# Kernel tuning notes

Hardware: AMD Instinct MI355X
Metric: run time of the kernel (lower is better)

Reference implementation:

```python
import jax, jax.numpy as jnp
import numpy as np

B, T, SLATE, D = 256, 16, 20, 256
N_ITEMS, N_USERS = 100000, 10000


def setup_inputs() -> dict:
    key = jax.random.key(0)
    ks = jax.random.split(key, 8)
    s = 1.0 / np.sqrt(D)  # PyTorch GRU/Linear init scale ~ U(-1/sqrt(H), 1/sqrt(H))
    return {
        "item_idxs": jax.random.randint(ks[0], (B, T, SLATE), 0, N_ITEMS),
        "user_idxs": jax.random.randint(ks[1], (B, T), 0, N_USERS),
        "responses": jnp.zeros((B, T, SLATE), jnp.float32),
        "item_table": jax.random.normal(ks[2], (N_ITEMS, D), jnp.float32) * 0.02,
        "user_table": jax.random.normal(ks[3], (N_USERS, D), jnp.float32) * 0.02,
        "W_ih": jax.random.uniform(ks[4], (3 * D, 2 * D), jnp.float32, -s, s),
        "W_hh": jax.random.uniform(ks[5], (3 * D, D), jnp.float32, -s, s),
        "b_ih": jnp.zeros((3 * D,), jnp.float32),
        "b_hh": jnp.zeros((3 * D,), jnp.float32),
        "W_out": jax.random.uniform(ks[6], (1, D), jnp.float32, -s, s),
        "b_out": jnp.zeros((1,), jnp.float32),
    }


def _gru_cell(x, h, W_ih, W_hh, b_ih, b_hh):
    # PyTorch GRUCell math. x: [N, 2D], h: [N, D]
    gi = x @ W_ih.T + b_ih  # [N, 3D]
    gh = h @ W_hh.T + b_hh  # [N, 3D]
    i_r, i_z, i_n = jnp.split(gi, 3, axis=-1)
    h_r, h_z, h_n = jnp.split(gh, 3, axis=-1)
    r = jax.nn.sigmoid(i_r + h_r)
    z = jax.nn.sigmoid(i_z + h_z)
    n = jnp.tanh(i_n + r * h_n)
    return (1.0 - z) * n + z * h


def reference(item_idxs, user_idxs, responses, item_table, user_table,
              W_ih, W_hh, b_ih, b_hh, W_out, b_out):
    # embedding lookup: item_embs [B,T,S,D], user_embs [B,T,D]
    item_embs = item_table[item_idxs]
    user_embs = user_table[user_idxs]
    N = B * T
    e = item_embs.reshape(N, SLATE, D).transpose(1, 0, 2)  # [S, N, D]
    h0 = user_embs.reshape(N, D)
    m0 = jnp.ones((N, 1), item_embs.dtype)  # 'soft' readout multiplier, 1 at step 0

    def step(carry, e_i):
        h, m = carry
        x = jnp.concatenate([e_i, e_i * m], axis=-1)  # [N, 2D]
        h = _gru_cell(x, h, W_ih, W_hh, b_ih, b_hh)
        y = h @ W_out.T + b_out  # [N, 1]
        return (h, jax.nn.sigmoid(y)), y[:, 0]

    _, ys = jax.lax.scan(step, (h0, m0), e)  # ys: [S, N]
    return ys.transpose(1, 0).reshape(B, T, SLATE)
```

## Files before the change

### kernel.cpp

```cpp
#include <hip/hip_runtime.h>
#include <math.h>

#define SLATE 20
#define DD 256
#define NSEQ 4096

typedef __attribute__((ext_vector_type(8))) short bf16x8;
typedef __attribute__((ext_vector_type(4))) float f32x4;
typedef unsigned short u16;
typedef unsigned int u32;

__device__ __forceinline__ u16 f2bf(float f) {
    unsigned u = __float_as_uint(f);
    u += 0x7fff + ((u >> 16) & 1);
    return (u16)(u >> 16);
}
__device__ __forceinline__ float blo(u32 u) { return __uint_as_float(u << 16); }
__device__ __forceinline__ float bhi(u32 u) { return __uint_as_float(u & 0xffff0000u); }
__device__ __forceinline__ float sigm_(float x) {
    return __builtin_amdgcn_rcpf(1.f + __builtin_amdgcn_exp2f(-1.44269504f * x));
}
__device__ __forceinline__ float tanh_(float x) {
    return 1.f - 2.f * __builtin_amdgcn_rcpf(1.f + __builtin_amdgcn_exp2f(2.88539008f * x));
}

__device__ __forceinline__ void gl_lds16(const void* g, void* l) {
    __builtin_amdgcn_global_load_lds(
        (const __attribute__((address_space(1))) unsigned int*)g,
        (__attribute__((address_space(3))) unsigned int*)l, 16, 0, 0);
}

__global__ void prep_w(const float* __restrict__ W_ih, const float* __restrict__ W_hh,
                       u16* __restrict__ W12, u16* __restrict__ Whh) {
    int i = blockIdx.x * 256 + threadIdx.x;
    if (i < 1536 * 256) {
        int j = i >> 8, k = i & 255;
        float v = (j < 768) ? W_ih[(size_t)j * 512 + k]
                            : W_ih[(size_t)(j - 768) * 512 + 256 + k];
        W12[i] = f2bf(v);
    } else {
        int i2 = i - 1536 * 256;
        Whh[i2] = f2bf(W_hh[i2]);
    }
}

__global__ void gather_e(int s0, const int* __restrict__ idxs, const float* __restrict__ itab,
                         u16* __restrict__ e_bf) {
    int g = blockIdx.x * 256 + threadIdx.x;
    int row = g >> 6, c = g & 63;
    int n = row & (NSEQ - 1), s = s0 + (row >> 12);
    int idx = idxs[n * SLATE + s];
    float4 v = *(const float4*)&itab[(size_t)idx * DD + c * 4];
    ushort4 o;
    o.x = f2bf(v.x); o.y = f2bf(v.y); o.z = f2bf(v.z); o.w = f2bf(v.w);
    *(ushort4*)&e_bf[(size_t)row * DD + c * 4] = o;
}

__global__ __launch_bounds__(256) void gemm_e(
        const u16* __restrict__ e_bf, const u16* __restrict__ W12,
        const float* __restrict__ b_ih, u16* __restrict__ Ge) {
    __shared__ u16 A_s[128][32];
    __shared__ u16 B_s[128][32];

    const int tid = threadIdx.x;
    const int w = tid >> 6, l = tid & 63, lm = l & 15, lq = l >> 4;
    const int wm = w & 1, wn = w >> 1;
    const size_t m0 = (size_t)blockIdx.y * 128;
    const size_t n0 = (size_t)blockIdx.x * 128;

    f32x4 acc[4][4];
    f32x4 zero4 = {0.f, 0.f, 0.f, 0.f};
#pragma unroll
    for (int mi = 0; mi < 4; ++mi)
#pragma unroll
        for (int nj = 0; nj < 4; ++nj) acc[mi][nj] = zero4;

    const int srow = w * 16 + (l >> 2);
    const int skc = (l & 3) * 8;
    const u16* gA = e_bf + (m0 + srow) * DD + skc;
    const u16* gB = W12 + (n0 + srow) * DD + skc;
    u16* lA = &A_s[0][0] + w * 512 + l * 8;
    u16* lB = &B_s[0][0] + w * 512 + l * 8;

    for (int kt = 0; kt < 8; ++kt) {
        const int ko = kt * 32;
        gl_lds16(gA + ko, lA);
        gl_lds16(gA + 64 * DD + ko, lA + 2048);
        gl_lds16(gB + ko, lB);
        gl_lds16(gB + 64 * DD + ko, lB + 2048);
        __syncthreads();
        bf16x8 af[4], bfr[4];
#pragma unroll
        for (int mi = 0; mi < 4; ++mi)
            af[mi] = *(const bf16x8*)&A_s[wm * 64 + mi * 16 + lm][lq * 8];
#pragma unroll
        for (int nj = 0; nj < 4; ++nj)
            bfr[nj] = *(const bf16x8*)&B_s[wn * 64 + nj * 16 + lm][lq * 8];
#pragma unroll
        for (int nj = 0; nj < 4; ++nj)
#pragma unroll
            for (int mi = 0; mi < 4; ++mi)
                acc[mi][nj] = __builtin_amdgcn_mfma_f32_16x16x32_bf16(af[mi], bfr[nj], acc[mi][nj], 0, 0, 0);
        __syncthreads();
    }
    float bb[4];
#pragma unroll
    for (int nj = 0; nj < 4; ++nj) {
        int col = (int)n0 + wn * 64 + nj * 16 + lm;
        bb[nj] = (col < 768) ? b_ih[col] : 0.f;
    }
#pragma unroll
    for (int mi = 0; mi < 4; ++mi)
#pragma unroll
        for (int rr = 0; rr < 4; ++rr) {
            u16* gp = Ge + (m0 + wm * 64 + mi * 16 + lq * 4 + rr) * 1536 + n0 + wn * 64 + lm;
#pragma unroll
            for (int nj = 0; nj < 4; ++nj) gp[nj * 16] = f2bf(acc[mi][nj][rr] + bb[nj]);
        }
}

__device__ __forceinline__ int hA_off(int seq, int kt, int lq2) {
    int v = ((kt & 3) << 2) | lq2;
    return kt * 512 + lq2 * 128 + ((seq ^ v) << 3);
}

__global__ __launch_bounds__(1024, 4) void seq_kernel(
        int s0, int C,
        const u16* __restrict__ Ge,
        const u16* __restrict__ Whh,
        const int* __restrict__ user_idxs, const float* __restrict__ user_table,
        const float* __restrict__ b_hh,
        const float* __restrict__ W_out, const float* __restrict__ b_out,
        float* __restrict__ h_g, float* __restrict__ m_g, float* __restrict__ out)
{
    __shared__ u16   hA[4096];
    __shared__ float gh_s[16][770];

    const int tid = threadIdx.x;
    const int w = tid >> 6, l = tid & 63, lm = l & 15, lq = l >> 4;
    const int n0 = blockIdx.x * 16;
    const int nw = n0 + w;
    const int jw = w * 48;

    const u16* wbase = Whh + (size_t)(jw + lm) * DD + lq * 8;
    bf16x8 warr0[8], warr1[8];
#pragma unroll
    for (int kt = 0; kt < 8; ++kt) {
        warr0[kt] = *(const bf16x8*)(wbase + kt * 32);
        warr1[kt] = *(const bf16x8*)(wbase + 16 * DD + kt * 32);
    }
    const u16* wb2 = wbase + 32 * DD;

    float bhh0 = b_hh[jw + lm], bhh1 = b_hh[jw + 16 + lm], bhh2 = b_hh[jw + 32 + lm];
    float2 woA = *(const float2*)&W_out[2 * l];
    float2 woB = *(const float2*)&W_out[2 * l + 128];
    const float bo = b_out[0];

    float h_reg[4]; float m_w;
    if (s0 == 0) {
        const float* hu = user_table + (size_t)user_idxs[nw] * DD;
        float2 a = *(const float2*)&hu[2 * l];
        float2 b = *(const float2*)&hu[2 * l + 128];
        h_reg[0] = a.x; h_reg[1] = a.y; h_reg[2] = b.x; h_reg[3] = b.y; m_w = 1.f;
    } else {
        float2 a = *(const float2*)&h_g[(size_t)nw * DD + 2 * l];
        float2 b = *(const float2*)&h_g[(size_t)nw * DD + 2 * l + 128];
        h_reg[0] = a.x; h_reg[1] = a.y; h_reg[2] = b.x; h_reg[3] = b.y; m_w = m_g[nw];
    }
#pragma unroll
    for (int c = 0; c < 2; ++c) {
        int kt = (l >> 4) + 4 * c, lq2 = (l >> 2) & 3;
        u32 pk = (u32)f2bf(h_reg[2 * c]) | ((u32)f2bf(h_reg[2 * c + 1]) << 16);
        *(u32*)&hA[hA_off(w, kt, lq2) + 2 * (l & 3)] = pk;
    }
    __syncthreads();

    for (int sc = 0; sc < C; ++sc) {
        u32 ge2[2][6];
        const u32* geb = (const u32*)(Ge + ((size_t)sc * NSEQ + nw) * 1536);
#pragma unroll
        for (int c = 0; c < 2; ++c)
#pragma unroll
            for (int g = 0; g < 6; ++g)
                ge2[c][g] = geb[g * 128 + l + 64 * c];

        f32x4 zero4 = {0.f, 0.f, 0.f, 0.f};
        f32x4 acc0 = zero4, acc1 = zero4, acc2 = zero4;
#pragma unroll
        for (int kt = 0; kt < 8; ++kt) {
            bf16x8 af = *(const bf16x8*)&hA[hA_off(lm, kt, lq)];
            acc0 = __builtin_amdgcn_mfma_f32_16x16x32_bf16(af, warr0[kt], acc0, 0, 0, 0);
            acc1 = __builtin_amdgcn_mfma_f32_16x16x32_bf16(af, warr1[kt], acc1, 0, 0, 0);
            bf16x8 b2 = *(const bf16x8*)(wb2 + kt * 32);
            acc2 = __builtin_amdgcn_mfma_f32_16x16x32_bf16(af, b2, acc2, 0, 0, 0);
        }
#pragma unroll
        for (int rr = 0; rr < 4; ++rr) {
            gh_s[lq * 4 + rr][jw + lm]      = acc0[rr] + bhh0;
            gh_s[lq * 4 + rr][jw + 16 + lm] = acc1[rr] + bhh1;
            gh_s[lq * 4 + rr][jw + 32 + lm] = acc2[rr] + bhh2;
        }
        __syncthreads();

        float yv = 0.f;
#pragma unroll
        for (int c = 0; c < 2; ++c) {
            const int d0 = 2 * l + 128 * c;
            float2 ghr = *(const float2*)&gh_s[w][d0];
            float2 ghz = *(const float2*)&gh_s[w][256 + d0];
            float2 ghn = *(const float2*)&gh_s[w][512 + d0];
            float ir_lo = fmaf(m_w, blo(ge2[c][3]), blo(ge2[c][0]));
            float ir_hi = fmaf(m_w, bhi(ge2[c][3]), bhi(ge2[c][0]));
            float iz_lo = fmaf(m_w, blo(ge2[c][4]), blo(ge2[c][1]));
            float iz_hi = fmaf(m_w, bhi(ge2[c][4]), bhi(ge2[c][1]));
            float in_lo = fmaf(m_w, blo(ge2[c][5]), blo(ge2[c][2]));
            float in_hi = fmaf(m_w, bhi(ge2[c][5]), bhi(ge2[c][2]));
            float r_lo = sigm_(ir_lo + ghr.x);
            float r_hi = sigm_(ir_hi + ghr.y);
            float z_lo = sigm_(iz_lo + ghz.x);
            float z_hi = sigm_(iz_hi + ghz.y);
            float n_lo = tanh_(fmaf(r_lo, ghn.x, in_lo));
            float n_hi = tanh_(fmaf(r_hi, ghn.y, in_hi));
            float hn_lo = fmaf(z_lo, h_reg[2 * c] - n_lo, n_lo);
            float hn_hi = fmaf(z_hi, h_reg[2 * c + 1] - n_hi, n_hi);
            h_reg[2 * c] = hn_lo; h_reg[2 * c + 1] = hn_hi;
            int kt = (l >> 4) + 4 * c, lq2 = (l >> 2) & 3;
            u32 pk = (u32)f2bf(hn_lo) | ((u32)f2bf(hn_hi) << 16);
            *(u32*)&hA[hA_off(w, kt, lq2) + 2 * (l & 3)] = pk;
            float2 wo2 = c ? woB : woA;
            yv += hn_lo * wo2.x + hn_hi * wo2.y;
        }
#pragma unroll
        for (int off = 32; off > 0; off >>= 1) yv += __shfl_xor(yv, off, 64);
        float y = yv + bo;
        if (l == 0) out[(size_t)nw * SLATE + (s0 + sc)] = y;
        m_w = sigm_(y);
        __syncthreads();
    }

#pragma unroll
    for (int c = 0; c < 2; ++c) {
        float2 v; v.x = h_reg[2 * c]; v.y = h_reg[2 * c + 1];
        *(float2*)&h_g[(size_t)nw * DD + 2 * l + 128 * c] = v;
    }
    if (l == 0) m_g[nw] = m_w;
}

extern "C" void kernel_launch(void* const* d_in, const int* in_sizes, int n_in,
                              void* d_out, int out_size, void* d_ws, size_t ws_size,
                              hipStream_t stream) {
    const int*   item_idxs  = (const int*)d_in[0];
    const int*   user_idxs  = (const int*)d_in[1];
    const float* item_table = (const float*)d_in[3];
    const float* user_table = (const float*)d_in[4];
    const float* W_ih       = (const float*)d_in[5];
    const float* W_hh       = (const float*)d_in[6];
    const float* b_ih       = (const float*)d_in[7];
    const float* b_hh       = (const float*)d_in[8];
    const float* W_out      = (const float*)d_in[9];
    const float* b_out      = (const float*)d_in[10];
    float* out = (float*)d_out;

    const size_t fixed = 786432ull + 393216ull + 4194304ull + 16384ull;
    static const int cands[5] = {10, 5, 4, 2, 1};
    int C = 1;
    for (int i = 0; i < 5; ++i) {
        size_t need = (size_t)cands[i] * (12582912ull + 2097152ull) + fixed;
        if (need <= ws_size) { C = cands[i]; break; }
    }

    u16*   Ge   = (u16*)d_ws;
    u16*   e_bf = (u16*)((char*)d_ws + (size_t)C * 12582912ull);
    u16*   W12  = (u16*)((char*)e_bf + (size_t)C * 2097152ull);
    u16*   Whh  = (u16*)((char*)W12 + 786432ull);
    float* h_g  = (float*)((char*)Whh + 393216ull);
    float* m_g  = (float*)((char*)h_g + 4194304ull);

    prep_w<<<2304, 256, 0, stream>>>(W_ih, W_hh, W12, Whh);

    for (int s0 = 0; s0 < SLATE; s0 += C) {
        gather_e<<<C * 1024, 256, 0, stream>>>(s0, item_idxs, item_table, e_bf);
        dim3 gg(12, 32 * C);
        gemm_e<<<gg, 256, 0, stream>>>(e_bf, W12, b_ih, Ge);
        seq_kernel<<<256, 1024, 0, stream>>>(s0, C, Ge, Whh, user_idxs, user_table,
                                             b_hh, W_out, b_out, h_g, m_g, out);
    }
}
```

Baseline: 442.8 us.

## Double-buffer per-step input-gate slices in LDS with async global-to-LDS prefetch

Replaces the per-step direct global loads of the precomputed input-gate values with a double-buffered LDS staging area. Each step issues asynchronous global-to-LDS copies for the next step while the recurrent MFMA and gate math for the current step run. The aim is to take global-load latency off the serial recurrence's critical path. In exchange it adds about 96 KB of LDS per block and relies on hand-written waitcnt/barrier sequences. The vmcnt(3) wait on the final iteration, where no new prefetch is issued, could let the step read data that has not fully arrived.

```diff
diff --git a/kernel.cpp b/kernel.cpp
--- a/kernel.cpp
+++ b/kernel.cpp
@@ -135,6 +135,7 @@
 {
     __shared__ u16   hA[4096];
     __shared__ float gh_s[16][770];
+    __shared__ u16   geL[2][16][1536];
 
     const int tid = threadIdx.x;
     const int w = tid >> 6, l = tid & 63, lm = l & 15, lq = l >> 4;
@@ -173,16 +174,22 @@
         u32 pk = (u32)f2bf(h_reg[2 * c]) | ((u32)f2bf(h_reg[2 * c + 1]) << 16);
         *(u32*)&hA[hA_off(w, kt, lq2) + 2 * (l & 3)] = pk;
     }
-    __syncthreads();
+
+    {
+        const u16* g0 = Ge + ((size_t)0 * NSEQ + n0) * 1536;
+        u16* l0 = &geL[0][0][0];
+#pragma unroll
+        for (int i = 0; i < 3; ++i) {
+            int ii = w + 16 * i;
+            gl_lds16(g0 + ii * 512 + l * 8, l0 + ii * 512);
+        }
+    }
+    asm volatile("s_waitcnt lgkmcnt(0)" ::: "memory");
+    __builtin_amdgcn_s_barrier();
+    __builtin_amdgcn_sched_barrier(0);
 
     for (int sc = 0; sc < C; ++sc) {
-        u32 ge2[2][6];
-        const u32* geb = (const u32*)(Ge + ((size_t)sc * NSEQ + nw) * 1536);
-#pragma unroll
-        for (int c = 0; c < 2; ++c)
-#pragma unroll
-            for (int g = 0; g < 6; ++g)
-                ge2[c][g] = geb[g * 128 + l + 64 * c];
+        const int cur = sc & 1;
 
         f32x4 zero4 = {0.f, 0.f, 0.f, 0.f};
         f32x4 acc0 = zero4, acc1 = zero4, acc2 = zero4;
@@ -194,13 +201,35 @@
             bf16x8 b2 = *(const bf16x8*)(wb2 + kt * 32);
             acc2 = __builtin_amdgcn_mfma_f32_16x16x32_bf16(af, b2, acc2, 0, 0, 0);
         }
+
+        __builtin_amdgcn_sched_barrier(0);
+        if (sc + 1 < C) {
+            const u16* gnx = Ge + ((size_t)(sc + 1) * NSEQ + n0) * 1536;
+            u16* lnx = &geL[cur ^ 1][0][0];
+#pragma unroll
+            for (int i = 0; i < 3; ++i) {
+                int ii = w + 16 * i;
+                gl_lds16(gnx + ii * 512 + l * 8, lnx + ii * 512);
+            }
+        }
+
 #pragma unroll
         for (int rr = 0; rr < 4; ++rr) {
             gh_s[lq * 4 + rr][jw + lm]      = acc0[rr] + bhh0;
             gh_s[lq * 4 + rr][jw + 16 + lm] = acc1[rr] + bhh1;
             gh_s[lq * 4 + rr][jw + 32 + lm] = acc2[rr] + bhh2;
         }
-        __syncthreads();
+        asm volatile("s_waitcnt vmcnt(3) lgkmcnt(0)" ::: "memory");
+        __builtin_amdgcn_s_barrier();
+        __builtin_amdgcn_sched_barrier(0);
+
+        const u32* grow = (const u32*)&geL[cur][w][0];
+        u32 ge2[2][6];
+#pragma unroll
+        for (int c = 0; c < 2; ++c)
+#pragma unroll
+            for (int g = 0; g < 6; ++g)
+                ge2[c][g] = grow[g * 128 + 64 * c + l];
 
         float yv = 0.f;
 #pragma unroll
@@ -235,7 +264,10 @@
         float y = yv + bo;
         if (l == 0) out[(size_t)nw * SLATE + (s0 + sc)] = y;
         m_w = sigm_(y);
-        __syncthreads();
+
+        asm volatile("s_waitcnt lgkmcnt(0)" ::: "memory");
+        __builtin_amdgcn_s_barrier();
+        __builtin_amdgcn_sched_barrier(0);
     }
 
 #pragma unroll
```

After: 445.8 us. No clear change (+0.7%).
